# Performance work log

Hardware: AMD Instinct MI355X
Metric: run time of the kernel (lower is better)

## Reference

```python
import jax, jax.numpy as jnp
import numpy as np

B, S, H, N, NREL = 16, 2048, 1024, 128, 8


def setup_inputs() -> dict:
    key = jax.random.key(0)
    ks = jax.random.split(key, 8)
    word_emb = jax.random.normal(ks[0], (B, S, H), dtype=jnp.float32)
    num_ids = jax.random.randint(ks[1], (B, N), 0, S)  # all valid (no -1 padding)
    is_response = jax.random.randint(ks[2], (B, N), 0, 2).astype(jnp.int32)
    numbers = jax.random.normal(ks[3], (B, N), dtype=jnp.float32)
    scale = 1.0 / np.sqrt(H).astype(np.float32)
    w_alpha = jax.random.normal(ks[4], (H, 1), dtype=jnp.float32) * scale
    b_alpha = jnp.zeros((1,), dtype=jnp.float32)
    w_f = jax.random.normal(ks[5], (H, H), dtype=jnp.float32) * scale
    b_f = jnp.zeros((H,), dtype=jnp.float32)
    W_r = jax.random.normal(ks[6], (NREL, H, H), dtype=jnp.float32) * scale  # 8 bias-free relation linears
    return dict(word_emb=word_emb, num_ids=num_ids, is_response=is_response,
                numbers=numbers, w_alpha=w_alpha, b_alpha=b_alpha,
                w_f=w_f, b_f=b_f, W_r=W_r)


def reference(word_emb, num_ids, is_response, numbers, w_alpha, b_alpha, w_f, b_f, W_r):
    Bn, Sn, Hn = word_emb.shape
    Nn = num_ids.shape[1]
    mask = (num_ids >= 0)  # [B,N] valid-node mask (original uses -1 padding)
    idx = jnp.clip(num_ids, 0, Sn - 1)
    # per-batch gather: Init[b,n] = word_emb[b, num_ids[b,n]]  -> [B,N,H]
    Init = jnp.take_along_axis(word_emb, idx[:, :, None], axis=1)
    alpha = jax.nn.sigmoid(Init @ w_alpha + b_alpha)  # [B,N,1]
    # all 8 relation transforms of every sender node j: T[b,r,j,:] = Init[b,j] @ W_r[r].T
    T = jnp.einsum('bnh,rkh->brnk', Init, W_r)  # [B,8,N,H]
    # relation id r(b,i,j) = 4*(num_i>num_j) + 2*resp_i + resp_j
    gt = (numbers[:, :, None] > numbers[:, None, :]).astype(jnp.int32)  # [B,N,N]
    resp = (is_response == 1).astype(jnp.int32)
    R = 4 * gt + 2 * resp[:, :, None] + resp[:, None, :]  # [B,N,N]
    sel = jax.nn.one_hot(R, NREL, dtype=word_emb.dtype)  # [B,N,N,8]
    not_diag = ~jnp.eye(Nn, dtype=bool)
    # edge weight over sender j: alpha_j, valid i & j, i != j
    wgt = (alpha[:, None, :, 0] * mask[:, None, :] * mask[:, :, None]
           * not_diag[None]).astype(word_emb.dtype)  # [B,N,N]
    Temp = jnp.einsum('bijr,brjh->bih', sel * wgt[..., None], T)  # [B,N,H]
    n_nodes = mask.sum(axis=1)  # [B]
    denom = jnp.maximum(n_nodes - 1, 1).astype(word_emb.dtype)
    Temp = Temp / denom[:, None, None]
    out = jax.nn.relu(Init @ w_f + b_f + Temp)  # [B,N,H]
    return out
```

## Files before the change

kernel.cpp:

```cpp
#include <hip/hip_runtime.h>
#include <hip/hip_bf16.h>
#include <stdint.h>

#define B_ 16
#define S_ 2048
#define H_ 1024
#define N_ 128
#define M_ (B_*N_)
#define K5 5120
#define MP 2176

typedef __attribute__((ext_vector_type(8))) short s8vec;
typedef __attribute__((ext_vector_type(4))) short s4vec;
typedef __attribute__((ext_vector_type(4))) float f4vec;
typedef __hip_bfloat16 bf16;

__global__ void k_sort(const int* __restrict__ num_ids, const int* __restrict__ is_resp,
                       const float* __restrict__ numbers,
                       int* __restrict__ sigma, int* __restrict__ newgrp,
                       int* __restrict__ respv, float* __restrict__ denom) {
    int b = blockIdx.x, i = threadIdx.x;
    __shared__ float nums[N_];
    __shared__ int sig[N_];
    __shared__ int cnt;
    float ni = numbers[b*N_ + i];
    int idv = num_ids[b*N_ + i];
    int valid = (idv >= 0) ? 1 : 0;
    nums[i] = ni;
    if (i == 0) cnt = 0;
    __syncthreads();
    int p = 0;
    for (int j = 0; j < N_; ++j) {
        float nj = nums[j];
        p += (nj < ni || (nj == ni && j < i)) ? 1 : 0;
    }
    sig[p] = i;
    atomicAdd(&cnt, valid);
    __syncthreads();
    sigma[b*N_ + i] = sig[i];
    int cur = sig[i];
    int prv = (i > 0) ? sig[i-1] : 0;
    newgrp[b*N_ + i] = (i == 0 || nums[cur] != nums[prv]) ? 1 : 0;
    respv[b*N_ + i] = ((is_resp[b*N_ + i] == 1) ? 1 : 0) | (valid << 1);
    if (i == 0) denom[b] = fmaxf((float)(cnt - 1), 1.0f);
}

__global__ void k_meta(const int* __restrict__ respv, int* __restrict__ aperm,
                       int* __restrict__ iperm, int* __restrict__ meta) {
    __shared__ int s0[1024], s1[1024];
    int t = threadIdx.x;
    aperm[t] = -1; aperm[t + 1024] = -1;
    if (t < MP - 2048) aperm[t + 2048] = -1;
    int r0 = 2*t, r1 = 2*t + 1;
    int c_a = respv[r0] & 1, c_b = respv[r1] & 1;
    int a0 = 1 - c_a, b0 = 1 - c_b;
    s0[t] = a0 + b0;
    s1[t] = c_a + c_b;
    __syncthreads();
    for (int off = 1; off < 1024; off <<= 1) {
        int v0 = (t >= off) ? s0[t-off] : 0;
        int v1 = (t >= off) ? s1[t-off] : 0;
        __syncthreads();
        s0[t] += v0; s1[t] += v1;
        __syncthreads();
    }
    int C0 = s0[1023], C1 = s1[1023];
    int P0 = ((C0 + 127) >> 7) << 7;
    int ex0 = s0[t] - (a0 + b0);
    int ex1 = s1[t] - (c_a + c_b);
    int p_a = (c_a == 0) ? ex0 : P0 + ex1;
    int p_b = (c_b == 0) ? ex0 + a0 : P0 + ex1 + c_a;
    aperm[p_a] = r0; iperm[r0] = p_a;
    aperm[p_b] = r1; iperm[r1] = p_b;
    if (t == 0) { meta[0] = P0; meta[1] = C0; meta[2] = C1; }
}

__global__ void k_gather(const float* __restrict__ word_emb, const int* __restrict__ num_ids,
                         const float* __restrict__ w_alpha, const float* __restrict__ b_alpha,
                         const float* __restrict__ denom, const int* __restrict__ iperm,
                         bf16* __restrict__ A, float* __restrict__ ascaled) {
    int blk = blockIdx.x;
    int b = blk >> 7, n = blk & 127;
    int t = threadIdx.x;
    int idv = num_ids[b*N_ + n];
    int valid = (idv >= 0) ? 1 : 0;
    int idx = idv < 0 ? 0 : (idv > S_-1 ? S_-1 : idv);
    int pr = iperm[b*N_ + n];
    const float4* row = (const float4*)(word_emb + ((size_t)b*S_ + idx)*H_);
    float4 v = row[t];
    float4 w = ((const float4*)w_alpha)[t];
    float part = v.x*w.x + v.y*w.y + v.z*w.z + v.w*w.w;
    union { s4vec v4; bf16 h[4]; } pk;
    pk.h[0] = __float2bfloat16(v.x);
    pk.h[1] = __float2bfloat16(v.y);
    pk.h[2] = __float2bfloat16(v.z);
    pk.h[3] = __float2bfloat16(v.w);
    *(s4vec*)(A + (size_t)pr*K5 + 4*H_ + t*4) = pk.v4;
#pragma unroll
    for (int off = 32; off > 0; off >>= 1) part += __shfl_down(part, off, 64);
    __shared__ float red[4];
    if ((t & 63) == 0) red[t >> 6] = part;
    __syncthreads();
    if (t == 0) {
        float dot = red[0] + red[1] + red[2] + red[3] + b_alpha[0];
        float al = 1.0f / (1.0f + __expf(-dot));
        ascaled[b*N_ + n] = valid ? (al / denom[b]) : 0.0f;
    }
}

__global__ void k_wt(const float* __restrict__ W_r, bf16* __restrict__ Wt) {
    size_t o = ((size_t)blockIdx.x*256 + threadIdx.x)*8;
    int cs = (int)(o >> 20);
    int c = cs >> 2, s = cs & 3;
    int r = ((s >> 1) << 2) + 2*c + (s & 1);
    size_t off = o & (size_t)(H_*H_ - 1);
    const float4* src = (const float4*)(W_r + (size_t)r*H_*H_ + off);
    float4 v0 = src[0], v1 = src[1];
    union { s8vec v8; bf16 h[8]; } pk;
    pk.h[0] = __float2bfloat16(v0.x); pk.h[1] = __float2bfloat16(v0.y);
    pk.h[2] = __float2bfloat16(v0.z); pk.h[3] = __float2bfloat16(v0.w);
    pk.h[4] = __float2bfloat16(v1.x); pk.h[5] = __float2bfloat16(v1.y);
    pk.h[6] = __float2bfloat16(v1.z); pk.h[7] = __float2bfloat16(v1.w);
    *(s8vec*)(Wt + (size_t)(c*5 + s)*H_*H_ + off) = pk.v8;
}

__global__ void k_wf(const float* __restrict__ w_f, bf16* __restrict__ Wt) {
    __shared__ float lds[64][65];
    int bi = blockIdx.x, bj = blockIdx.y;
    int t = threadIdx.x;
    int ty = t >> 4, tx = t & 15;
#pragma unroll
    for (int i = 0; i < 4; ++i) {
        int r = ty*4 + i;
        float4 v = *(const float4*)(w_f + (size_t)(bi*64 + r)*H_ + bj*64 + tx*4);
        lds[r][tx*4+0] = v.x; lds[r][tx*4+1] = v.y;
        lds[r][tx*4+2] = v.z; lds[r][tx*4+3] = v.w;
    }
    __syncthreads();
    bf16* d0 = Wt + (size_t)4*H_*H_;
    bf16* d1 = Wt + (size_t)9*H_*H_;
#pragma unroll
    for (int i = 0; i < 4; ++i) {
        int n = ty*4 + i;
        size_t doff = (size_t)(bj*64 + n)*H_ + bi*64 + tx*4;
        union { s4vec v4; bf16 h[4]; } pk;
#pragma unroll
        for (int j = 0; j < 4; ++j) pk.h[j] = __float2bfloat16(lds[tx*4+j][n]);
        *(s4vec*)(d0 + doff) = pk.v4;
        *(s4vec*)(d1 + doff) = pk.v4;
    }
}

__global__ void k_build(const float* __restrict__ ascaled, const int* __restrict__ sigma,
                        const int* __restrict__ newgrp, const int* __restrict__ respv,
                        const int* __restrict__ iperm, bf16* __restrict__ A) {
    int b = blockIdx.y;
    int h = blockIdx.x*64 + threadIdx.x;
    __shared__ float as_s[N_];
    __shared__ int sig_s[N_], ng_s[N_], rv_s[N_], pm_s[N_];
    for (int j = threadIdx.x; j < N_; j += 64) {
        as_s[j] = ascaled[b*N_ + j];
        sig_s[j] = sigma[b*N_ + j];
        ng_s[j] = newgrp[b*N_ + j];
        rv_s[j] = respv[b*N_ + j];
        pm_s[j] = iperm[b*N_ + j];
    }
    __syncthreads();
    const bf16* initcol = A + 4*H_ + h;
    float tot0 = 0.f, tot1 = 0.f;
    for (int i2 = 0; i2 < N_; ++i2) {
        float v = as_s[i2] * __bfloat162float(initcol[(size_t)pm_s[i2]*K5]);
        if (rv_s[i2] & 1) tot1 += v; else tot0 += v;
    }
    float cS0=0.f, cS1=0.f, cG0=0.f, cG1=0.f;
    for (int p = 0; p < N_; ++p) {
        int i2 = sig_s[p];
        if (ng_s[p]) { cS0 += cG0; cS1 += cG1; cG0 = 0.f; cG1 = 0.f; }
        float v = as_s[i2] * __bfloat162float(initcol[(size_t)pm_s[i2]*K5]);
        int resp = rv_s[i2] & 1;
        float vf = (rv_s[i2] >> 1) ? 1.0f : 0.0f;
        float G0 = cS0, G1 = cS1;
        float L0 = tot0 - G0 - (resp ? 0.f : v);
        float L1 = tot1 - G1 - (resp ? v : 0.f);
        bf16* Ar = A + (size_t)pm_s[i2]*K5 + h;
        Ar[0*H_] = __float2bfloat16(L0*vf);
        Ar[1*H_] = __float2bfloat16(L1*vf);
        Ar[2*H_] = __float2bfloat16(G0*vf);
        Ar[3*H_] = __float2bfloat16(G1*vf);
        if (resp) cG1 += v; else cG0 += v;
    }
}

#define BM 128
#define BN 128
#define BK 64
#define NSTEP (K5/BK)

__global__ __launch_bounds__(256) void k_gemm(const bf16* __restrict__ A,
                                              const bf16* __restrict__ Wt,
                                              const int* __restrict__ meta,
                                              const int* __restrict__ aperm,
                                              const float* __restrict__ b_f,
                                              float* __restrict__ out) {
    __shared__ __align__(16) bf16 As0[BM*BK], As1[BM*BK];
    __shared__ __align__(16) bf16 Bs0[BN*BK], Bs1[BN*BK];
    int tid = threadIdx.x;
    int w = tid >> 6, lane = tid & 63;
    int q = lane >> 4, r = lane & 15;
    int bid = blockIdx.x;
    int wg = (bid & 7)*17 + (bid >> 3);
    int mt = wg % 17, nt = wg / 17;
    int rowBase = mt * BM, colBase = nt * BN;
    int wm = w >> 1, wn = w & 1;
    int P0 = meta[0];
    const bf16* Wtc = Wt + ((rowBase >= P0) ? (size_t)5*H_*H_ : 0);

    f4vec acc[4][4];
#pragma unroll
    for (int mi = 0; mi < 4; ++mi)
#pragma unroll
        for (int ni = 0; ni < 4; ++ni)
#pragma unroll
            for (int e = 0; e < 4; ++e) acc[mi][ni][e] = 0.0f;

    auto STAGE = [&](bf16* AsB, bf16* BsB, int kin) {
        int slot = kin >> 10, koff = kin & 1023;
        const bf16* Wslot = Wtc + ((size_t)slot << 20);
#pragma unroll
        for (int j = 0; j < 4; ++j) {
            int c = tid + j*256;
            int row = c >> 3;
            int p = (c & 7) ^ (row & 7);
            const bf16* ga = A + (size_t)(rowBase + row)*K5 + kin + p*8;
            __builtin_amdgcn_global_load_lds((const __attribute__((address_space(1))) void*)ga,
                (__attribute__((address_space(3))) void*)((char*)AsB + j*4096 + w*1024), 16, 0, 0);
            const bf16* gb = Wslot + ((size_t)(colBase + row) << 10) + koff + p*8;
            __builtin_amdgcn_global_load_lds((const __attribute__((address_space(1))) void*)gb,
                (__attribute__((address_space(3))) void*)((char*)BsB + j*4096 + w*1024), 16, 0, 0);
        }
    };

    auto COMPUTE = [&](const bf16* AsB, const bf16* BsB) {
        const short* Asp = (const short*)AsB;
        const short* Bsp = (const short*)BsB;
        s8vec af[2][4], bfr[2][4];
#pragma unroll
        for (int kk = 0; kk < 2; ++kk) {
            int sl = ((kk*4 + q) ^ (r & 7)) << 3;
#pragma unroll
            for (int mi = 0; mi < 4; ++mi)
                af[kk][mi] = *(const s8vec*)(Asp + (wm*64 + mi*16 + r)*BK + sl);
#pragma unroll
            for (int ni = 0; ni < 4; ++ni)
                bfr[kk][ni] = *(const s8vec*)(Bsp + (wn*64 + ni*16 + r)*BK + sl);
        }
#pragma unroll
        for (int kk = 0; kk < 2; ++kk)
#pragma unroll
            for (int mi = 0; mi < 4; ++mi)
#pragma unroll
                for (int ni = 0; ni < 4; ++ni)
                    acc[mi][ni] = __builtin_amdgcn_mfma_f32_16x16x32_bf16(
                        af[kk][mi], bfr[kk][ni], acc[mi][ni], 0, 0, 0);
    };

    STAGE(As0, Bs0, 0);
    for (int t = 0; t < NSTEP; t += 2) {
        __syncthreads();
        if (t + 1 < NSTEP) STAGE(As1, Bs1, (t+1)*BK);
        COMPUTE(As0, Bs0);
        __syncthreads();
        if (t + 2 < NSTEP) STAGE(As0, Bs0, (t+2)*BK);
        COMPUTE(As1, Bs1);
    }

    float bias[4];
#pragma unroll
    for (int ni = 0; ni < 4; ++ni) bias[ni] = b_f[colBase + wn*64 + ni*16 + r];
#pragma unroll
    for (int mi = 0; mi < 4; ++mi) {
        int rb = rowBase + wm*64 + mi*16 + q*4;
        int og0 = aperm[rb+0], og1 = aperm[rb+1], og2 = aperm[rb+2], og3 = aperm[rb+3];
#pragma unroll
        for (int ni = 0; ni < 4; ++ni) {
            int cc = colBase + wn*64 + ni*16 + r;
            if (og0 >= 0) out[(size_t)og0*H_ + cc] = fmaxf(acc[mi][ni][0] + bias[ni], 0.0f);
            if (og1 >= 0) out[(size_t)og1*H_ + cc] = fmaxf(acc[mi][ni][1] + bias[ni], 0.0f);
            if (og2 >= 0) out[(size_t)og2*H_ + cc] = fmaxf(acc[mi][ni][2] + bias[ni], 0.0f);
            if (og3 >= 0) out[(size_t)og3*H_ + cc] = fmaxf(acc[mi][ni][3] + bias[ni], 0.0f);
        }
    }
}

extern "C" void kernel_launch(void* const* d_in, const int* in_sizes, int n_in,
                              void* d_out, int out_size, void* d_ws, size_t ws_size,
                              hipStream_t stream) {
    (void)in_sizes; (void)n_in; (void)out_size; (void)ws_size;
    const float* word_emb = (const float*)d_in[0];
    const int*   num_ids  = (const int*)d_in[1];
    const int*   is_resp  = (const int*)d_in[2];
    const float* numbers  = (const float*)d_in[3];
    const float* w_alpha  = (const float*)d_in[4];
    const float* b_alpha  = (const float*)d_in[5];
    const float* w_f      = (const float*)d_in[6];
    const float* b_f      = (const float*)d_in[7];
    const float* W_r      = (const float*)d_in[8];
    float* out = (float*)d_out;

    char* ws = (char*)d_ws;
    bf16*  Aws     = (bf16*)(ws);
    bf16*  Wt      = (bf16*)(ws + 22282240);
    float* ascaled = (float*)(ws + 52166656);
    int*   sigma   = (int*)(ws + 52174848);
    int*   newgrp  = (int*)(ws + 52183040);
    int*   respv   = (int*)(ws + 52191232);
    float* denom   = (float*)(ws + 52199424);
    int*   aperm   = (int*)(ws + 52199488);
    int*   iperm   = (int*)(ws + 52208192);
    int*   meta    = (int*)(ws + 52216384);

    k_sort  <<<16,   128, 0, stream>>>(num_ids, is_resp, numbers, sigma, newgrp, respv, denom);
    k_meta  <<<1,   1024, 0, stream>>>(respv, aperm, iperm, meta);
    k_gather<<<2048, 256, 0, stream>>>(word_emb, num_ids, w_alpha, b_alpha, denom, iperm,
                                       Aws, ascaled);
    k_wt    <<<4096, 256, 0, stream>>>(W_r, Wt);
    k_wf    <<<dim3(16,16), 256, 0, stream>>>(w_f, Wt);
    k_build <<<dim3(16,16), 64, 0, stream>>>(ascaled, sigma, newgrp, respv, iperm, Aws);
    k_gemm  <<<136,  256, 0, stream>>>(Aws, Wt, meta, aperm, b_f, out);
}
```

Baseline: 346.3 us.

## Shrink GEMM tiles to 64x64 with triple-buffered pipeline and fuse weight-convert kernels

The GEMM moves from 128x128 to 64x64 tiles, which quadruples the grid from 136 to 544 blocks so more CUs are busy. It replaces double buffering with a three-stage LDS ring that uses explicit vmcnt waits and a single barrier per step, and it hoists the aperm and bias loads ahead of the main loop. The two weight-conversion kernels are merged into one launch, and the loops in k_build get unroll pragmas. Smaller tiles cut per-block reuse and raise global/L2 traffic for A and W, in exchange for better occupancy and latency hiding.

Measured after the change: 322.4 us. 6.9% less time.

```diff
diff --git a/kernel.cpp b/kernel.cpp
--- a/kernel.cpp
+++ b/kernel.cpp
@@ -108,26 +108,29 @@
     }
 }
 
-__global__ void k_wt(const float* __restrict__ W_r, bf16* __restrict__ Wt) {
-    size_t o = ((size_t)blockIdx.x*256 + threadIdx.x)*8;
-    int cs = (int)(o >> 20);
-    int c = cs >> 2, s = cs & 3;
-    int r = ((s >> 1) << 2) + 2*c + (s & 1);
-    size_t off = o & (size_t)(H_*H_ - 1);
-    const float4* src = (const float4*)(W_r + (size_t)r*H_*H_ + off);
-    float4 v0 = src[0], v1 = src[1];
-    union { s8vec v8; bf16 h[8]; } pk;
-    pk.h[0] = __float2bfloat16(v0.x); pk.h[1] = __float2bfloat16(v0.y);
-    pk.h[2] = __float2bfloat16(v0.z); pk.h[3] = __float2bfloat16(v0.w);
-    pk.h[4] = __float2bfloat16(v1.x); pk.h[5] = __float2bfloat16(v1.y);
-    pk.h[6] = __float2bfloat16(v1.z); pk.h[7] = __float2bfloat16(v1.w);
-    *(s8vec*)(Wt + (size_t)(c*5 + s)*H_*H_ + off) = pk.v8;
-}
-
-__global__ void k_wf(const float* __restrict__ w_f, bf16* __restrict__ Wt) {
+__global__ void k_wtf(const float* __restrict__ W_r, const float* __restrict__ w_f,
+                      bf16* __restrict__ Wt) {
     __shared__ float lds[64][65];
-    int bi = blockIdx.x, bj = blockIdx.y;
+    int bid = blockIdx.x;
     int t = threadIdx.x;
+    if (bid < 4096) {
+        size_t o = ((size_t)bid*256 + t)*8;
+        int cs = (int)(o >> 20);
+        int c = cs >> 2, s = cs & 3;
+        int r = ((s >> 1) << 2) + 2*c + (s & 1);
+        size_t off = o & (size_t)(H_*H_ - 1);
+        const float4* src = (const float4*)(W_r + (size_t)r*H_*H_ + off);
+        float4 v0 = src[0], v1 = src[1];
+        union { s8vec v8; bf16 h[8]; } pk;
+        pk.h[0] = __float2bfloat16(v0.x); pk.h[1] = __float2bfloat16(v0.y);
+        pk.h[2] = __float2bfloat16(v0.z); pk.h[3] = __float2bfloat16(v0.w);
+        pk.h[4] = __float2bfloat16(v1.x); pk.h[5] = __float2bfloat16(v1.y);
+        pk.h[6] = __float2bfloat16(v1.z); pk.h[7] = __float2bfloat16(v1.w);
+        *(s8vec*)(Wt + (size_t)(c*5 + s)*H_*H_ + off) = pk.v8;
+        return;
+    }
+    int bb = bid - 4096;
+    int bi = bb & 15, bj = bb >> 4;
     int ty = t >> 4, tx = t & 15;
 #pragma unroll
     for (int i = 0; i < 4; ++i) {
@@ -168,11 +171,13 @@
     __syncthreads();
     const bf16* initcol = A + 4*H_ + h;
     float tot0 = 0.f, tot1 = 0.f;
+#pragma unroll 8
     for (int i2 = 0; i2 < N_; ++i2) {
         float v = as_s[i2] * __bfloat162float(initcol[(size_t)pm_s[i2]*K5]);
         if (rv_s[i2] & 1) tot1 += v; else tot0 += v;
     }
     float cS0=0.f, cS1=0.f, cG0=0.f, cG1=0.f;
+#pragma unroll 8
     for (int p = 0; p < N_; ++p) {
         int i2 = sig_s[p];
         if (ng_s[p]) { cS0 += cG0; cS1 += cG1; cG0 = 0.f; cG1 = 0.f; }
@@ -191,35 +196,51 @@
     }
 }
 
-#define BM 128
-#define BN 128
+#define BM 64
+#define BN 64
 #define BK 64
 #define NSTEP (K5/BK)
 
-__global__ __launch_bounds__(256) void k_gemm(const bf16* __restrict__ A,
-                                              const bf16* __restrict__ Wt,
-                                              const int* __restrict__ meta,
-                                              const int* __restrict__ aperm,
-                                              const float* __restrict__ b_f,
-                                              float* __restrict__ out) {
-    __shared__ __align__(16) bf16 As0[BM*BK], As1[BM*BK];
-    __shared__ __align__(16) bf16 Bs0[BN*BK], Bs1[BN*BK];
+__global__ __launch_bounds__(256, 3) void k_gemm(const bf16* __restrict__ A,
+                                                 const bf16* __restrict__ Wt,
+                                                 const int* __restrict__ meta,
+                                                 const int* __restrict__ aperm,
+                                                 const float* __restrict__ b_f,
+                                                 float* __restrict__ out) {
+    __shared__ __align__(16) bf16 As0[BM*BK], As1[BM*BK], As2[BM*BK];
+    __shared__ __align__(16) bf16 Bs0[BN*BK], Bs1[BN*BK], Bs2[BN*BK];
     int tid = threadIdx.x;
     int w = tid >> 6, lane = tid & 63;
     int q = lane >> 4, r = lane & 15;
     int bid = blockIdx.x;
-    int wg = (bid & 7)*17 + (bid >> 3);
-    int mt = wg % 17, nt = wg / 17;
+    int wg = (bid & 7)*68 + (bid >> 3);
+    int mt = wg % 34, nt = wg / 34;
     int rowBase = mt * BM, colBase = nt * BN;
     int wm = w >> 1, wn = w & 1;
     int P0 = meta[0];
     const bf16* Wtc = Wt + ((rowBase >= P0) ? (size_t)5*H_*H_ : 0);
 
-    f4vec acc[4][4];
-#pragma unroll
-    for (int mi = 0; mi < 4; ++mi)
-#pragma unroll
-        for (int ni = 0; ni < 4; ++ni)
+    int og[2][4];
+    float bias[2];
+#pragma unroll
+    for (int mi = 0; mi < 2; ++mi) {
+        int rb = rowBase + wm*32 + mi*16 + q*4;
+#pragma unroll
+        for (int e = 0; e < 4; ++e) og[mi][e] = aperm[rb + e];
+    }
+#pragma unroll
+    for (int ni = 0; ni < 2; ++ni) bias[ni] = b_f[colBase + wn*32 + ni*16 + r];
+#pragma unroll
+    for (int mi = 0; mi < 2; ++mi)
+#pragma unroll
+        for (int e = 0; e < 4; ++e) asm volatile("" : "+v"(og[mi][e]));
+    asm volatile("" : "+v"(bias[0]), "+v"(bias[1]));
+
+    f4vec acc[2][2];
+#pragma unroll
+    for (int mi = 0; mi < 2; ++mi)
+#pragma unroll
+        for (int ni = 0; ni < 2; ++ni)
 #pragma unroll
             for (int e = 0; e < 4; ++e) acc[mi][ni][e] = 0.0f;
 
@@ -227,7 +248,7 @@
         int slot = kin >> 10, koff = kin & 1023;
         const bf16* Wslot = Wtc + ((size_t)slot << 20);
 #pragma unroll
-        for (int j = 0; j < 4; ++j) {
+        for (int j = 0; j < 2; ++j) {
             int c = tid + j*256;
             int row = c >> 3;
             int p = (c & 7) ^ (row & 7);
@@ -243,51 +264,52 @@
     auto COMPUTE = [&](const bf16* AsB, const bf16* BsB) {
         const short* Asp = (const short*)AsB;
         const short* Bsp = (const short*)BsB;
-        s8vec af[2][4], bfr[2][4];
+        s8vec af[2][2], bfr[2][2];
 #pragma unroll
         for (int kk = 0; kk < 2; ++kk) {
             int sl = ((kk*4 + q) ^ (r & 7)) << 3;
 #pragma unroll
-            for (int mi = 0; mi < 4; ++mi)
-                af[kk][mi] = *(const s8vec*)(Asp + (wm*64 + mi*16 + r)*BK + sl);
-#pragma unroll
-            for (int ni = 0; ni < 4; ++ni)
-                bfr[kk][ni] = *(const s8vec*)(Bsp + (wn*64 + ni*16 + r)*BK + sl);
+            for (int mi = 0; mi < 2; ++mi)
+                af[kk][mi] = *(const s8vec*)(Asp + (wm*32 + mi*16 + r)*BK + sl);
+#pragma unroll
+            for (int ni = 0; ni < 2; ++ni)
+                bfr[kk][ni] = *(const s8vec*)(Bsp + (wn*32 + ni*16 + r)*BK + sl);
         }
 #pragma unroll
         for (int kk = 0; kk < 2; ++kk)
 #pragma unroll
-            for (int mi = 0; mi < 4; ++mi)
-#pragma unroll
-                for (int ni = 0; ni < 4; ++ni)
+            for (int mi = 0; mi < 2; ++mi)
+#pragma unroll
+                for (int ni = 0; ni < 2; ++ni)
                     acc[mi][ni] = __builtin_amdgcn_mfma_f32_16x16x32_bf16(
                         af[kk][mi], bfr[kk][ni], acc[mi][ni], 0, 0, 0);
     };
 
     STAGE(As0, Bs0, 0);
-    for (int t = 0; t < NSTEP; t += 2) {
-        __syncthreads();
-        if (t + 1 < NSTEP) STAGE(As1, Bs1, (t+1)*BK);
-        COMPUTE(As0, Bs0);
-        __syncthreads();
-        if (t + 2 < NSTEP) STAGE(As0, Bs0, (t+2)*BK);
-        COMPUTE(As1, Bs1);
-    }
-
-    float bias[4];
-#pragma unroll
-    for (int ni = 0; ni < 4; ++ni) bias[ni] = b_f[colBase + wn*64 + ni*16 + r];
-#pragma unroll
-    for (int mi = 0; mi < 4; ++mi) {
-        int rb = rowBase + wm*64 + mi*16 + q*4;
-        int og0 = aperm[rb+0], og1 = aperm[rb+1], og2 = aperm[rb+2], og3 = aperm[rb+3];
-#pragma unroll
-        for (int ni = 0; ni < 4; ++ni) {
-            int cc = colBase + wn*64 + ni*16 + r;
-            if (og0 >= 0) out[(size_t)og0*H_ + cc] = fmaxf(acc[mi][ni][0] + bias[ni], 0.0f);
-            if (og1 >= 0) out[(size_t)og1*H_ + cc] = fmaxf(acc[mi][ni][1] + bias[ni], 0.0f);
-            if (og2 >= 0) out[(size_t)og2*H_ + cc] = fmaxf(acc[mi][ni][2] + bias[ni], 0.0f);
-            if (og3 >= 0) out[(size_t)og3*H_ + cc] = fmaxf(acc[mi][ni][3] + bias[ni], 0.0f);
+    STAGE(As1, Bs1, BK);
+    bf16 *cA = As0, *cB = Bs0;
+    bf16 *nA = As1, *nB = Bs1;
+    bf16 *sA = As2, *sB = Bs2;
+    for (int t = 0; t < NSTEP; ++t) {
+        if (t + 1 < NSTEP) asm volatile("s_waitcnt vmcnt(4)" ::: "memory");
+        else               asm volatile("s_waitcnt vmcnt(0)" ::: "memory");
+        __builtin_amdgcn_s_barrier();
+        __builtin_amdgcn_sched_barrier(0);
+        if (t + 2 < NSTEP) STAGE(sA, sB, (t + 2)*BK);
+        COMPUTE(cA, cB);
+        bf16* tA = cA; cA = nA; nA = sA; sA = tA;
+        bf16* tB = cB; cB = nB; nB = sB; sB = tB;
+    }
+
+#pragma unroll
+    for (int mi = 0; mi < 2; ++mi) {
+#pragma unroll
+        for (int ni = 0; ni < 2; ++ni) {
+            int cc = colBase + wn*32 + ni*16 + r;
+            if (og[mi][0] >= 0) out[(size_t)og[mi][0]*H_ + cc] = fmaxf(acc[mi][ni][0] + bias[ni], 0.0f);
+            if (og[mi][1] >= 0) out[(size_t)og[mi][1]*H_ + cc] = fmaxf(acc[mi][ni][1] + bias[ni], 0.0f);
+            if (og[mi][2] >= 0) out[(size_t)og[mi][2]*H_ + cc] = fmaxf(acc[mi][ni][2] + bias[ni], 0.0f);
+            if (og[mi][3] >= 0) out[(size_t)og[mi][3]*H_ + cc] = fmaxf(acc[mi][ni][3] + bias[ni], 0.0f);
         }
     }
 }
@@ -323,8 +345,7 @@
     k_meta  <<<1,   1024, 0, stream>>>(respv, aperm, iperm, meta);
     k_gather<<<2048, 256, 0, stream>>>(word_emb, num_ids, w_alpha, b_alpha, denom, iperm,
                                        Aws, ascaled);
-    k_wt    <<<4096, 256, 0, stream>>>(W_r, Wt);
-    k_wf    <<<dim3(16,16), 256, 0, stream>>>(w_f, Wt);
+    k_wtf   <<<4352, 256, 0, stream>>>(W_r, w_f, Wt);
     k_build <<<dim3(16,16), 64, 0, stream>>>(ascaled, sigma, newgrp, respv, iperm, Aws);
-    k_gemm  <<<136,  256, 0, stream>>>(Aws, Wt, meta, aperm, b_f, out);
-}
+    k_gemm  <<<544,  256, 0, stream>>>(Aws, Wt, meta, aperm, b_f, out);
+}
```
